# Performance work log

Hardware: AMD Instinct MI355X
Metric: run time of the kernel (lower is better)

Reference implementation:

```python
import jax, jax.numpy as jnp
import numpy as np
import math

D_MODEL = 1024
N_HEAD = 16
FFN_HIDDEN = 4096
EPS = 1e-12


def _layernorm(x, gamma, beta):
    # faithful to repo: unbiased std (ddof=1), divide by (std + eps)
    mean = jnp.mean(x, axis=-1, keepdims=True)
    std = jnp.std(x, axis=-1, keepdims=True, ddof=1)
    return gamma * ((x - mean) / (std + EPS)) + beta


def setup_inputs() -> dict:
    key = jax.random.key(0)
    ks = jax.random.split(key, 12)
    B, L, D, H = 2, 2048, D_MODEL, FFN_HIDDEN
    s = 0.02
    inp = {
        "x": jax.random.normal(ks[0], (B, L, D), dtype=jnp.float32),
        "src_mask": jnp.ones((B, 1, 1, L), dtype=jnp.int32),
        "wq_w": jax.random.normal(ks[1], (D, D), jnp.float32) * s,
        "wq_b": jnp.zeros((D,), jnp.float32),
        "wk_w": jax.random.normal(ks[2], (D, D), jnp.float32) * s,
        "wk_b": jnp.zeros((D,), jnp.float32),
        "wv_w": jax.random.normal(ks[3], (D, D), jnp.float32) * s,
        "wv_b": jnp.zeros((D,), jnp.float32),
        "wo_w": jax.random.normal(ks[4], (D, D), jnp.float32) * s,
        "wo_b": jnp.zeros((D,), jnp.float32),
        "gamma1": jnp.ones((D,), jnp.float32),
        "beta1": jnp.zeros((D,), jnp.float32),
        "ff1_w": jax.random.normal(ks[5], (D, H), jnp.float32) * s,
        "ff1_b": jnp.zeros((H,), jnp.float32),
        "ff2_w": jax.random.normal(ks[6], (H, D), jnp.float32) * s,
        "ff2_b": jnp.zeros((D,), jnp.float32),
        "gamma2": jnp.ones((D,), jnp.float32),
        "beta2": jnp.zeros((D,), jnp.float32),
    }
    return inp


def _encoder_layer(x, src_mask, wq_w, wq_b, wk_w, wk_b, wv_w, wv_b, wo_w, wo_b,
                   gamma1, beta1, ff1_w, ff1_b, ff2_w, ff2_b, gamma2, beta2):
    B, L, D = x.shape
    H = N_HEAD
    d_t = D // H
    # projections
    q = x @ wq_w + wq_b
    k = x @ wk_w + wk_b
    v = x @ wv_w + wv_b
    # faithful .view() split: reshape [B,L,D] -> [B,H,L,d_t] (no transpose)
    q = q.reshape(B, H, L, d_t)
    k = k.reshape(B, H, L, d_t)
    v = v.reshape(B, H, L, d_t)
    score = jnp.einsum("bhqd,bhkd->bhqk", q, k) / math.sqrt(d_t)
    score = jnp.where(src_mask == 0, jnp.float32(-1e-12), score)
    score = jax.nn.softmax(score, axis=-1)
    out = jnp.einsum("bhqk,bhkd->bhqd", score, v)
    out = out.reshape(B, L, D)  # faithful .view() concat
    attn = out @ wo_w + wo_b
    # residual + LN1 (dropout p=0)
    x1 = _layernorm(attn + x, gamma1, beta1)
    # FFN
    ff = jax.nn.relu(x1 @ ff1_w + ff1_b) @ ff2_w + ff2_b
    return _layernorm(ff + x1, gamma2, beta2)


def reference(x, src_mask, wq_w, wq_b, wk_w, wk_b, wv_w, wv_b, wo_w, wo_b,
              gamma1, beta1, ff1_w, ff1_b, ff2_w, ff2_b, gamma2, beta2):
    return _encoder_layer(x, src_mask, wq_w, wq_b, wk_w, wk_b, wv_w, wv_b,
                          wo_w, wo_b, gamma1, beta1, ff1_w, ff1_b, ff2_w,
                          ff2_b, gamma2, beta2)
```

## Files before the change

### kernel.cpp

```cpp
#include <hip/hip_runtime.h>
#include <hip/hip_bf16.h>
#include <cstdint>
#include <cstddef>

using bf16 = __hip_bfloat16;
typedef __attribute__((ext_vector_type(8))) short short8v;
typedef __attribute__((ext_vector_type(4))) short short4v;
typedef __attribute__((ext_vector_type(4))) float float4v;

__device__ inline float b2f(short s) {
  union { float f; uint32_t u; } z; z.u = ((uint32_t)(uint16_t)s) << 16; return z.f;
}
__device__ inline short f2b(float f) {
  bf16 h = __float2bfloat16(f);
  return *reinterpret_cast<short*>(&h);
}

typedef const __attribute__((address_space(1))) uint32_t* gas1p;
typedef __attribute__((address_space(3))) uint32_t* las3p;
__device__ inline void gload_lds16(const void* g, void* l) {
  __builtin_amdgcn_global_load_lds((gas1p)g, (las3p)l, 16, 0, 0);
}

__global__ __launch_bounds__(256) void gemm_bt(
    const bf16* __restrict__ A, const bf16* __restrict__ Bt,
    const float* __restrict__ bias, void* __restrict__ C,
    int M, int N, int K, int ldc, int relu_mode, int out_f32) {
  __shared__ __align__(16) bf16 As[128 * 32];
  __shared__ __align__(16) bf16 Bs[128 * 32];
  const int tid = threadIdx.x;
  const int w = tid >> 6, lane = tid & 63;
  const int quad = lane >> 4, l16 = lane & 15;
  const int wrow = (w >> 1) * 64, wcol = (w & 1) * 64;
  const int mbase = blockIdx.y * 128, nbase = blockIdx.x * 128;
  const int c = w * 128 + lane;
  const int row0 = c >> 2, p0 = c & 3;
  const int row1 = (c + 64) >> 2, p1 = (c + 64) & 3;

  float4v acc[4][4];
  for (int i = 0; i < 4; i++)
    for (int j = 0; j < 4; j++) acc[i][j] = (float4v){0.f, 0.f, 0.f, 0.f};

  for (int k0 = 0; k0 < K; k0 += 32) {
    __syncthreads();
    gload_lds16(A + (size_t)(mbase + row0) * K + k0 + p0 * 8, (char*)As + w * 2048);
    gload_lds16(A + (size_t)(mbase + row1) * K + k0 + p1 * 8, (char*)As + w * 2048 + 1024);
    gload_lds16(Bt + (size_t)(nbase + row0) * K + k0 + p0 * 8, (char*)Bs + w * 2048);
    gload_lds16(Bt + (size_t)(nbase + row1) * K + k0 + p1 * 8, (char*)Bs + w * 2048 + 1024);
    __syncthreads();

    short8v a[4], b[4];
    for (int mt = 0; mt < 4; mt++)
      a[mt] = *reinterpret_cast<const short8v*>(As + (wrow + mt * 16 + l16) * 32 + quad * 8);
    for (int nt = 0; nt < 4; nt++)
      b[nt] = *reinterpret_cast<const short8v*>(Bs + (wcol + nt * 16 + l16) * 32 + quad * 8);
    for (int mt = 0; mt < 4; mt++)
      for (int nt = 0; nt < 4; nt++)
        acc[mt][nt] = __builtin_amdgcn_mfma_f32_16x16x32_bf16(a[mt], b[nt], acc[mt][nt], 0, 0, 0);
  }

  for (int nt = 0; nt < 4; nt++) {
    int col = nbase + wcol + nt * 16 + l16;
    float bv = bias[col];
    for (int mt = 0; mt < 4; mt++) {
      int row = mbase + wrow + mt * 16 + quad * 4;
      for (int r = 0; r < 4; r++) {
        float v = acc[mt][nt][r] + bv;
        if (relu_mode) v = fmaxf(v, 0.f);
        size_t idx = (size_t)(row + r) * ldc + col;
        if (out_f32) ((float*)C)[idx] = v;
        else         ((short*)C)[idx] = f2b(v);
      }
    }
  }
}

__global__ __launch_bounds__(256) void gemm_pipe(
    const bf16* __restrict__ A, const bf16* __restrict__ Bt,
    float* __restrict__ C, int K, int ldc, int k_len) {
  __shared__ __align__(16) bf16 As[2][128 * 32];
  __shared__ __align__(16) bf16 Bs[2][128 * 32];
  const int tid = threadIdx.x;
  const int w = tid >> 6, lane = tid & 63;
  const int quad = lane >> 4, l16 = lane & 15;
  const int wrow = (w >> 1) * 64, wcol = (w & 1) * 64;
  const int mbase = blockIdx.y * 128, nbase = blockIdx.x * 128;
  const int srow = tid >> 1, scol = (tid & 1) * 16;

  const bf16* ag = A + (size_t)(mbase + srow) * K + blockIdx.z * k_len + scol;
  const bf16* bg = Bt + (size_t)(nbase + srow) * K + blockIdx.z * k_len + scol;

  float4v acc[4][4];
  for (int i = 0; i < 4; i++)
    for (int j = 0; j < 4; j++) acc[i][j] = (float4v){0.f, 0.f, 0.f, 0.f};

  {
    short8v a0 = *reinterpret_cast<const short8v*>(ag);
    short8v a1 = *reinterpret_cast<const short8v*>(ag + 8);
    short8v b0 = *reinterpret_cast<const short8v*>(bg);
    short8v b1 = *reinterpret_cast<const short8v*>(bg + 8);
    *reinterpret_cast<short8v*>(&As[0][srow * 32 + scol])     = a0;
    *reinterpret_cast<short8v*>(&As[0][srow * 32 + scol + 8]) = a1;
    *reinterpret_cast<short8v*>(&Bs[0][srow * 32 + scol])     = b0;
    *reinterpret_cast<short8v*>(&Bs[0][srow * 32 + scol + 8]) = b1;
  }
  __syncthreads();

  const int KT = k_len >> 5;
  for (int kt = 0; kt < KT; kt++) {
    const int pb = kt & 1;
    short8v na0, na1, nb0, nb1;
    const bool more = (kt + 1 < KT);
    if (more) {
      const bf16* ap = ag + (kt + 1) * 32;
      const bf16* bp = bg + (kt + 1) * 32;
      na0 = *reinterpret_cast<const short8v*>(ap);
      na1 = *reinterpret_cast<const short8v*>(ap + 8);
      nb0 = *reinterpret_cast<const short8v*>(bp);
      nb1 = *reinterpret_cast<const short8v*>(bp + 8);
    }

    short8v a[4], b[4];
    for (int mt = 0; mt < 4; mt++)
      a[mt] = *reinterpret_cast<const short8v*>(&As[pb][(wrow + mt * 16 + l16) * 32 + quad * 8]);
    for (int nt = 0; nt < 4; nt++)
      b[nt] = *reinterpret_cast<const short8v*>(&Bs[pb][(wcol + nt * 16 + l16) * 32 + quad * 8]);
    for (int mt = 0; mt < 4; mt++)
      for (int nt = 0; nt < 4; nt++)
        acc[mt][nt] = __builtin_amdgcn_mfma_f32_16x16x32_bf16(a[mt], b[nt], acc[mt][nt], 0, 0, 0);

    if (more) {
      *reinterpret_cast<short8v*>(&As[1 - pb][srow * 32 + scol])     = na0;
      *reinterpret_cast<short8v*>(&As[1 - pb][srow * 32 + scol + 8]) = na1;
      *reinterpret_cast<short8v*>(&Bs[1 - pb][srow * 32 + scol])     = nb0;
      *reinterpret_cast<short8v*>(&Bs[1 - pb][srow * 32 + scol + 8]) = nb1;
    }
    __syncthreads();
  }

  for (int nt = 0; nt < 4; nt++) {
    int col = nbase + wcol + nt * 16 + l16;
    for (int mt = 0; mt < 4; mt++) {
      int row = mbase + wrow + mt * 16 + quad * 4;
      for (int r = 0; r < 4; r++)
        atomicAdd(&C[(size_t)(row + r) * ldc + col], acc[mt][nt][r]);
    }
  }
}

__global__ __launch_bounds__(256) void bias_init(
    const float* __restrict__ bias, float* __restrict__ C) {
  int c = threadIdx.x * 4;
  float4 bv = *reinterpret_cast<const float4*>(bias + c);
  *reinterpret_cast<float4*>(C + (size_t)blockIdx.x * 1024 + c) = bv;
}

__global__ __launch_bounds__(256) void attn_kernel(
    const bf16* __restrict__ qkv, const int* __restrict__ mask,
    bf16* __restrict__ ao) {
  __shared__ __align__(16) short Vt[2][64 * 40];
  __shared__ __align__(16) short Pbuf[4][32 * 40];

  const int tid = threadIdx.x;
  const int w = tid >> 6, lane = tid & 63;
  const int quad = lane >> 4, l16 = lane & 15;
  const int bh = blockIdx.y, b = bh >> 4;
  const int row0 = bh * 128;
  const int qbase = blockIdx.x * 128 + w * 32;
  const int vr = tid & 31, vdb = (tid >> 5) * 8;

  short8v aq[2][2];
  for (int h = 0; h < 2; h++)
    for (int dh = 0; dh < 2; dh++) {
      int local = (qbase + h * 16 + l16) * 64 + dh * 32 + quad * 8;
      aq[h][dh] = *reinterpret_cast<const short8v*>(
          qkv + (size_t)(row0 + (local >> 10)) * 3072 + (local & 1023));
    }

  const bf16* pk[2][2];
  for (int s = 0; s < 2; s++)
    for (int dh = 0; dh < 2; dh++) {
      int local = (s * 16 + l16) * 64 + dh * 32 + quad * 8;
      pk[s][dh] = qkv + (size_t)(row0 + (local >> 10)) * 3072 + (local & 1023) + 1024;
    }
  const bf16* pv;
  {
    int local = vr * 64 + vdb;
    pv = qkv + (size_t)(row0 + (local >> 10)) * 3072 + (local & 1023) + 2048;
  }
  const int* pm = mask + b * 2048 + quad * 4;

  float4v o[2][4];
  for (int h = 0; h < 2; h++)
    for (int nt = 0; nt < 4; nt++) o[h][nt] = (float4v){0.f, 0.f, 0.f, 0.f};
  float lsum[2] = {0.f, 0.f};

  short8v kcur[2][2], vcur;
  vcur = *reinterpret_cast<const short8v*>(pv);
  for (int s = 0; s < 2; s++)
    for (int dh = 0; dh < 2; dh++)
      kcur[s][dh] = *reinterpret_cast<const short8v*>(pk[s][dh]);
  int4 mc0 = *reinterpret_cast<const int4*>(pm);
  int4 mc1 = *reinterpret_cast<const int4*>(pm + 16);
  pv += 6144; pm += 32;
  for (int s = 0; s < 2; s++)
    for (int dh = 0; dh < 2; dh++) pk[s][dh] += 6144;
  {
    short* vt = &Vt[0][0];
    for (int j = 0; j < 8; j++) vt[(vdb + j) * 40 + vr] = vcur[j];
  }
  __syncthreads();

  for (int it = 0; it < 64; it++) {
    const int pb = it & 1;
    short8v knext[2][2], vnext;
    int4 mn0, mn1;
    if (it < 63) {
      vnext = *reinterpret_cast<const short8v*>(pv);
      for (int s = 0; s < 2; s++)
        for (int dh = 0; dh < 2; dh++)
          knext[s][dh] = *reinterpret_cast<const short8v*>(pk[s][dh]);
      mn0 = *reinterpret_cast<const int4*>(pm);
      mn1 = *reinterpret_cast<const int4*>(pm + 16);
      pv += 6144; pm += 32;
      for (int s = 0; s < 2; s++)
        for (int dh = 0; dh < 2; dh++) pk[s][dh] += 6144;
    }

    float4v st[2][2];
    for (int s = 0; s < 2; s++)
      for (int h = 0; h < 2; h++) {
        float4v t = (float4v){0.f, 0.f, 0.f, 0.f};
        t = __builtin_amdgcn_mfma_f32_16x16x32_bf16(kcur[s][0], aq[h][0], t, 0, 0, 0);
        t = __builtin_amdgcn_mfma_f32_16x16x32_bf16(kcur[s][1], aq[h][1], t, 0, 0, 0);
        st[s][h] = t;
      }

    for (int h = 0; h < 2; h++)
      for (int s = 0; s < 2; s++) {
        int4 mv = s ? mc1 : mc0;
        int mm[4] = {mv.x, mv.y, mv.z, mv.w};
        short4v pkv;
        for (int r = 0; r < 4; r++) {
          float y = st[s][h][r] * 0.180336880f;
          y = fminf(fmaxf(y, -43.3f), 43.3f);
          y = (mm[r] == 0) ? -1.4427e-12f : y;
          float e = __builtin_amdgcn_exp2f(y);
          lsum[h] += e;
          pkv[r] = f2b(e);
        }
        *reinterpret_cast<short4v*>(&Pbuf[w][(h * 16 + l16) * 40 + s * 16 + quad * 4]) = pkv;
      }
    short8v pf[2];
    for (int h = 0; h < 2; h++)
      pf[h] = *reinterpret_cast<const short8v*>(&Pbuf[w][(h * 16 + l16) * 40 + quad * 8]);
    for (int nt = 0; nt < 4; nt++) {
      short8v bv = *reinterpret_cast<const short8v*>(&Vt[pb][(nt * 16 + l16) * 40 + quad * 8]);
      for (int h = 0; h < 2; h++)
        o[h][nt] = __builtin_amdgcn_mfma_f32_16x16x32_bf16(pf[h], bv, o[h][nt], 0, 0, 0);
    }

    if (it < 63) {
      short* vt = &Vt[1 - pb][0];
      for (int j = 0; j < 8; j++) vt[(vdb + j) * 40 + vr] = vnext[j];
      for (int s = 0; s < 2; s++)
        for (int dh = 0; dh < 2; dh++) kcur[s][dh] = knext[s][dh];
      mc0 = mn0; mc1 = mn1;
    }
    __syncthreads();
  }

  for (int h = 0; h < 2; h++) {
    lsum[h] += __shfl_xor(lsum[h], 16);
    lsum[h] += __shfl_xor(lsum[h], 32);
  }
  for (int h = 0; h < 2; h++)
    for (int r = 0; r < 4; r++) {
      float linv = 1.0f / __shfl(lsum[h], quad * 4 + r);
      int qg = qbase + h * 16 + quad * 4 + r;
      for (int nt = 0; nt < 4; nt++) {
        int d = nt * 16 + l16;
        ao[(size_t)bh * 131072 + (size_t)qg * 64 + d] = __float2bfloat16(o[h][nt][r] * linv);
      }
    }
}

__global__ __launch_bounds__(256) void ln_resid(
    const void* __restrict__ a, const void* __restrict__ xres,
    const float* __restrict__ gamma, const float* __restrict__ beta,
    void* __restrict__ out, int a_f32, int x_f32, int out_f32) {
  __shared__ float red[8];
  const int row = blockIdx.x, tid = threadIdx.x;
  const int w = tid >> 6, lane = tid & 63;
  const size_t base = (size_t)row * 1024;
  float v[4]; float sum = 0.f, ss = 0.f;
  for (int i = 0; i < 4; i++) {
    int c = tid + i * 256;
    float av = a_f32 ? ((const float*)a)[base + c] : b2f(((const short*)a)[base + c]);
    float xv = x_f32 ? ((const float*)xres)[base + c] : b2f(((const short*)xres)[base + c]);
    v[i] = av + xv;
    sum += v[i]; ss += v[i] * v[i];
  }
  for (int off = 1; off < 64; off <<= 1) {
    sum += __shfl_xor(sum, off);
    ss  += __shfl_xor(ss, off);
  }
  if (lane == 0) { red[w * 2] = sum; red[w * 2 + 1] = ss; }
  __syncthreads();
  sum = red[0] + red[2] + red[4] + red[6];
  ss  = red[1] + red[3] + red[5] + red[7];
  float mean = sum * (1.0f / 1024.0f);
  float var = (ss - 1024.0f * mean * mean) * (1.0f / 1023.0f);
  var = fmaxf(var, 0.f);
  float rden = 1.0f / (sqrtf(var) + 1e-12f);
  for (int i = 0; i < 4; i++) {
    int c = tid + i * 256;
    float y = gamma[c] * ((v[i] - mean) * rden) + beta[c];
    if (out_f32) ((float*)out)[base + c] = y;
    else         ((short*)out)[base + c] = f2b(y);
  }
}

__global__ __launch_bounds__(256) void transpose_k(
    const float* __restrict__ in, bf16* __restrict__ out, int R, int C) {
  __shared__ short t[32][33];
  const int tx = threadIdx.x, ty = threadIdx.y;
  const int cb = blockIdx.x * 32, rb = blockIdx.y * 32;
  for (int j = 0; j < 4; j++)
    t[ty + j * 8][tx] = f2b(in[(size_t)(rb + ty + j * 8) * C + cb + tx]);
  __syncthreads();
  for (int j = 0; j < 4; j++)
    ((short*)out)[(size_t)(cb + ty + j * 8) * R + rb + tx] = t[tx][ty + j * 8];
}

__global__ __launch_bounds__(256) void concat3(
    const float* __restrict__ a, const float* __restrict__ b,
    const float* __restrict__ c, float* __restrict__ out) {
  int i = blockIdx.x * 256 + threadIdx.x;
  float v;
  if (i < 1024)       v = a[i];
  else if (i < 2048)  v = b[i - 1024];
  else                v = c[i - 2048];
  out[i] = v;
}

__global__ __launch_bounds__(256) void cast_f32_bf16(
    const float* __restrict__ in, bf16* __restrict__ out) {
  int i0 = (blockIdx.x * 256 + threadIdx.x) * 4;
  float4 f = *reinterpret_cast<const float4*>(in + i0);
  short* o = (short*)out + i0;
  o[0] = f2b(f.x); o[1] = f2b(f.y); o[2] = f2b(f.z); o[3] = f2b(f.w);
}

extern "C" void kernel_launch(void* const* d_in, const int* in_sizes, int n_in,
                              void* d_out, int out_size, void* d_ws, size_t ws_size,
                              hipStream_t stream) {
  (void)in_sizes; (void)n_in; (void)out_size; (void)ws_size;
  const float* x    = (const float*)d_in[0];
  const int*   mask = (const int*)d_in[1];
  const float* wq_w = (const float*)d_in[2];
  const float* wq_b = (const float*)d_in[3];
  const float* wk_w = (const float*)d_in[4];
  const float* wk_b = (const float*)d_in[5];
  const float* wv_w = (const float*)d_in[6];
  const float* wv_b = (const float*)d_in[7];
  const float* wo_w = (const float*)d_in[8];
  const float* wo_b = (const float*)d_in[9];
  const float* g1   = (const float*)d_in[10];
  const float* be1  = (const float*)d_in[11];
  const float* f1w  = (const float*)d_in[12];
  const float* f1b  = (const float*)d_in[13];
  const float* f2w  = (const float*)d_in[14];
  const float* f2b_ = (const float*)d_in[15];
  const float* g2   = (const float*)d_in[16];
  const float* be2  = (const float*)d_in[17];
  float* out = (float*)d_out;
  char* ws = (char*)d_ws;

  bf16*  QKV  = (bf16*)(ws + 0);
  bf16*  Xbf  = (bf16*)(ws + 25165824);
  bf16*  AO   = (bf16*)(ws + 25165824);
  float* PROJ = (float*)(ws + 0);
  bf16*  H    = (bf16*)(ws + 0);
  bf16*  X1   = (bf16*)(ws + 33554432);
  bf16*  WT   = (bf16*)(ws + 41943040);
  float* BQKV = (float*)(ws + 48234496);

  dim3 tb(32, 8);
  cast_f32_bf16<<<dim3(4096), dim3(256), 0, stream>>>(x, Xbf);
  transpose_k<<<dim3(32, 32), tb, 0, stream>>>(wq_w, WT, 1024, 1024);
  transpose_k<<<dim3(32, 32), tb, 0, stream>>>(wk_w, WT + 1024 * 1024, 1024, 1024);
  transpose_k<<<dim3(32, 32), tb, 0, stream>>>(wv_w, WT + 2 * 1024 * 1024, 1024, 1024);
  concat3<<<dim3(12), dim3(256), 0, stream>>>(wq_b, wk_b, wv_b, BQKV);
  gemm_bt<<<dim3(24, 32), dim3(256), 0, stream>>>(Xbf, WT, BQKV, QKV, 4096, 3072, 1024, 3072, 0, 0);
  attn_kernel<<<dim3(16, 32), dim3(256), 0, stream>>>(QKV, mask, AO);
  transpose_k<<<dim3(32, 32), tb, 0, stream>>>(wo_w, WT, 1024, 1024);
  bias_init<<<dim3(4096), dim3(256), 0, stream>>>(wo_b, PROJ);
  gemm_pipe<<<dim3(8, 32, 2), dim3(256), 0, stream>>>(AO, WT, PROJ, 1024, 1024, 512);
  ln_resid<<<dim3(4096), dim3(256), 0, stream>>>(PROJ, x, g1, be1, X1, 1, 1, 0);
  transpose_k<<<dim3(128, 32), tb, 0, stream>>>(f1w, WT, 1024, 4096);
  gemm_bt<<<dim3(32, 32), dim3(256), 0, stream>>>(X1, WT, f1b, H, 4096, 4096, 1024, 4096, 1, 0);
  transpose_k<<<dim3(32, 128), tb, 0, stream>>>(f2w, WT, 4096, 1024);
  bias_init<<<dim3(4096), dim3(256), 0, stream>>>(f2b_, out);
  gemm_pipe<<<dim3(8, 32, 2), dim3(256), 0, stream>>>(H, WT, out, 4096, 1024, 2048);
  ln_resid<<<dim3(4096), dim3(256), 0, stream>>>(out, X1, g2, be2, out, 1, 0, 1);
}
```

Measured before the change: 473.6 us.

## Split attention KV range across two blocks and add combine kernel

The attention kernel gets a grid z dimension of 2, so each block processes half of the key/value sequence, doubling the block count for better CU occupancy. Each half writes unnormalized bf16 partial outputs and row sums to workspace. A new combine kernel adds the partials and divides by the total sum. This costs extra memory traffic, an extra launch and bf16 rounding of partials. The exp-argument clamp is also removed to shave ALU work, which risks overflow on large scores.

```diff
diff --git a/kernel.cpp b/kernel.cpp
--- a/kernel.cpp
+++ b/kernel.cpp
@@ -157,7 +157,7 @@
 
 __global__ __launch_bounds__(256) void attn_kernel(
     const bf16* __restrict__ qkv, const int* __restrict__ mask,
-    bf16* __restrict__ ao) {
+    bf16* __restrict__ po, float* __restrict__ lbuf) {
   __shared__ __align__(16) short Vt[2][64 * 40];
   __shared__ __align__(16) short Pbuf[4][32 * 40];
 
@@ -165,6 +165,8 @@
   const int w = tid >> 6, lane = tid & 63;
   const int quad = lane >> 4, l16 = lane & 15;
   const int bh = blockIdx.y, b = bh >> 4;
+  const int z = blockIdx.z;
+  const int kvbase = z * 1024;
   const int row0 = bh * 128;
   const int qbase = blockIdx.x * 128 + w * 32;
   const int vr = tid & 31, vdb = (tid >> 5) * 8;
@@ -180,15 +182,15 @@
   const bf16* pk[2][2];
   for (int s = 0; s < 2; s++)
     for (int dh = 0; dh < 2; dh++) {
-      int local = (s * 16 + l16) * 64 + dh * 32 + quad * 8;
+      int local = (kvbase + s * 16 + l16) * 64 + dh * 32 + quad * 8;
       pk[s][dh] = qkv + (size_t)(row0 + (local >> 10)) * 3072 + (local & 1023) + 1024;
     }
   const bf16* pv;
   {
-    int local = vr * 64 + vdb;
+    int local = (kvbase + vr) * 64 + vdb;
     pv = qkv + (size_t)(row0 + (local >> 10)) * 3072 + (local & 1023) + 2048;
   }
-  const int* pm = mask + b * 2048 + quad * 4;
+  const int* pm = mask + b * 2048 + kvbase + quad * 4;
 
   float4v o[2][4];
   for (int h = 0; h < 2; h++)
@@ -211,11 +213,11 @@
   }
   __syncthreads();
 
-  for (int it = 0; it < 64; it++) {
+  for (int it = 0; it < 32; it++) {
     const int pb = it & 1;
     short8v knext[2][2], vnext;
     int4 mn0, mn1;
-    if (it < 63) {
+    if (it < 31) {
       vnext = *reinterpret_cast<const short8v*>(pv);
       for (int s = 0; s < 2; s++)
         for (int dh = 0; dh < 2; dh++)
@@ -243,7 +245,6 @@
         short4v pkv;
         for (int r = 0; r < 4; r++) {
           float y = st[s][h][r] * 0.180336880f;
-          y = fminf(fmaxf(y, -43.3f), 43.3f);
           y = (mm[r] == 0) ? -1.4427e-12f : y;
           float e = __builtin_amdgcn_exp2f(y);
           lsum[h] += e;
@@ -260,7 +261,7 @@
         o[h][nt] = __builtin_amdgcn_mfma_f32_16x16x32_bf16(pf[h], bv, o[h][nt], 0, 0, 0);
     }
 
-    if (it < 63) {
+    if (it < 31) {
       short* vt = &Vt[1 - pb][0];
       for (int j = 0; j < 8; j++) vt[(vdb + j) * 40 + vr] = vnext[j];
       for (int s = 0; s < 2; s++)
@@ -274,15 +275,32 @@
     lsum[h] += __shfl_xor(lsum[h], 16);
     lsum[h] += __shfl_xor(lsum[h], 32);
   }
+  bf16* pop = po + (size_t)z * 4194304 + (size_t)bh * 131072;
+  float* lp = lbuf + z * 65536 + bh * 2048;
   for (int h = 0; h < 2; h++)
     for (int r = 0; r < 4; r++) {
-      float linv = 1.0f / __shfl(lsum[h], quad * 4 + r);
+      float lv = __shfl(lsum[h], quad * 4 + r);
       int qg = qbase + h * 16 + quad * 4 + r;
+      if (l16 == 0) lp[qg] = lv;
       for (int nt = 0; nt < 4; nt++) {
         int d = nt * 16 + l16;
-        ao[(size_t)bh * 131072 + (size_t)qg * 64 + d] = __float2bfloat16(o[h][nt][r] * linv);
+        pop[(size_t)qg * 64 + d] = __float2bfloat16(o[h][nt][r]);
       }
     }
+}
+
+__global__ __launch_bounds__(256) void attn_combine(
+    const bf16* __restrict__ po, const float* __restrict__ lbuf,
+    bf16* __restrict__ ao) {
+  int i4 = (blockIdx.x * 256 + threadIdx.x) * 4;
+  int row = i4 >> 6;
+  float linv = 1.0f / (lbuf[row] + lbuf[65536 + row]);
+  short4v p0 = *reinterpret_cast<const short4v*>((const short*)po + i4);
+  short4v p1 = *reinterpret_cast<const short4v*>((const short*)po + 4194304 + i4);
+  short4v ov;
+  for (int j = 0; j < 4; j++)
+    ov[j] = f2b((b2f(p0[j]) + b2f(p1[j])) * linv);
+  *reinterpret_cast<short4v*>((short*)ao + i4) = ov;
 }
 
 __global__ __launch_bounds__(256) void ln_resid(
@@ -379,8 +397,10 @@
 
   bf16*  QKV  = (bf16*)(ws + 0);
   bf16*  Xbf  = (bf16*)(ws + 25165824);
-  bf16*  AO   = (bf16*)(ws + 25165824);
-  float* PROJ = (float*)(ws + 0);
+  bf16*  Po   = (bf16*)(ws + 25165824);
+  float* Lb   = (float*)(ws + 41943040);
+  bf16*  AO   = (bf16*)(ws + 0);
+  float* PROJ = (float*)(ws + 8388608);
   bf16*  H    = (bf16*)(ws + 0);
   bf16*  X1   = (bf16*)(ws + 33554432);
   bf16*  WT   = (bf16*)(ws + 41943040);
@@ -393,7 +413,8 @@
   transpose_k<<<dim3(32, 32), tb, 0, stream>>>(wv_w, WT + 2 * 1024 * 1024, 1024, 1024);
   concat3<<<dim3(12), dim3(256), 0, stream>>>(wq_b, wk_b, wv_b, BQKV);
   gemm_bt<<<dim3(24, 32), dim3(256), 0, stream>>>(Xbf, WT, BQKV, QKV, 4096, 3072, 1024, 3072, 0, 0);
-  attn_kernel<<<dim3(16, 32), dim3(256), 0, stream>>>(QKV, mask, AO);
+  attn_kernel<<<dim3(16, 32, 2), dim3(256), 0, stream>>>(QKV, mask, Po, Lb);
+  attn_combine<<<dim3(4096), dim3(256), 0, stream>>>(Po, Lb, AO);
   transpose_k<<<dim3(32, 32), tb, 0, stream>>>(wo_w, WT, 1024, 1024);
   bias_init<<<dim3(4096), dim3(256), 0, stream>>>(wo_b, PROJ);
   gemm_pipe<<<dim3(8, 32, 2), dim3(256), 0, stream>>>(AO, WT, PROJ, 1024, 1024, 512);
```

Result: slower. 493.1 us (+4.1%).
